# Performance work log

Measured on AMD Instinct MI355X. Metric: run time of the kernel, lower is better.

The kernel has to match this reference:

```python
import jax, jax.numpy as jnp
import numpy as np

B, T, C, H = 4, 4096, 1024, 64  # batch, seq_len, n_embd, head_size


def setup_inputs() -> dict:
    key = jax.random.key(0)
    kx, kk, kq, kv = jax.random.split(key, 4)
    x = jax.random.normal(kx, (B, T, C), dtype=jnp.float32)
    Wk = jax.random.normal(kk, (C, H), dtype=jnp.float32) * (C ** -0.5)
    Wq = jax.random.normal(kq, (C, H), dtype=jnp.float32) * (C ** -0.5)
    Wv = jax.random.normal(kv, (C, H), dtype=jnp.float32) * (C ** -0.5)
    return {"x": x, "Wk": Wk, "Wq": Wq, "Wv": Wv}


def reference(x, Wk, Wq, Wv):
    # q,k,v: (B,T,H)
    k = jnp.einsum('btc,ch->bth', x, Wk)
    q = jnp.einsum('btc,ch->bth', x, Wq)
    v = jnp.einsum('btc,ch->bth', x, Wv)
    # NOTE: source scales by C**-0.5 (embedding dim), not head_size**-0.5
    scale = jnp.asarray(C, x.dtype) ** -0.5
    scores = jnp.einsum('bqh,bkh->bqk', q, k) * scale  # (B,T,T)
    causal = jnp.tril(jnp.ones((T, T), dtype=bool))
    scores = jnp.where(causal, scores, jnp.asarray(-jnp.inf, scores.dtype))
    weight = jax.nn.softmax(scores, axis=-1)
    out = jnp.einsum('bqk,bkh->bqh', weight, v)  # (B,T,H)
    return out
```

## Files before the change

kernel.cpp:

```cpp
#include <hip/hip_runtime.h>

typedef unsigned short u16;
typedef unsigned int u32;
typedef float v4f __attribute__((ext_vector_type(4)));
typedef __bf16 v8bf __attribute__((ext_vector_type(8)));

__device__ __forceinline__ u16 f2bf(float f) {
    union { float f; u32 u; } v; v.f = f;
    u32 r = v.u + 0x7fffu + ((v.u >> 16) & 1u);
    return (u16)(r >> 16);
}
__device__ __forceinline__ u32 pk2(float lo, float hi) {
    return ((u32)f2bf(hi) << 16) | (u32)f2bf(lo);
}
__device__ __forceinline__ u32 pk2t(float lo, float hi) {
    union { float f; u32 u; } a, b; a.f = hi; b.f = lo;
    return __builtin_amdgcn_perm(a.u, b.u, 0x07060302u);
}
__device__ __forceinline__ v4f zero4() { v4f z = {0.f, 0.f, 0.f, 0.f}; return z; }

__global__ __launch_bounds__(64) void prep_w(const float* __restrict__ Wk,
                                             const float* __restrict__ Wq,
                                             const float* __restrict__ Wv,
                                             u16* __restrict__ WtF) {
    const int f = blockIdx.x >> 5;
    const int ks = blockIdx.x & 31;
    const int lane = threadIdx.x;
    const int w = f >> 2;
    const float* W = (w == 0) ? Wk : ((w == 1) ? Wq : Wv);
    const int h = (f & 3) * 16 + (lane & 15);
    const int k0 = ks * 32 + (lane >> 4) * 8;
    u16 tmp[8];
#pragma unroll
    for (int j = 0; j < 8; ++j) tmp[j] = f2bf(W[(size_t)(k0 + j) * 64 + h]);
    *(uint4*)&WtF[((size_t)blockIdx.x * 64 + lane) * 8] = *(const uint4*)tmp;
}

__global__ __launch_bounds__(256, 4) void qkv_proj(const float* __restrict__ x,
                                                   const u16* __restrict__ WtF,
                                                   u16* __restrict__ qg,
                                                   u16* __restrict__ Kf,
                                                   u16* __restrict__ Vf) {
    __shared__ v4f red[3][12][64];
    u16* Tk = (u16*)&red[0][0][0];
    u16* Tq = Tk + 16 * 72;
    u16* Tv = Tq + 16 * 72;

    const int tid = threadIdx.x;
    const int lane = tid & 63;
    const int wv = tid >> 6;
    const int l15 = lane & 15, quad = lane >> 4;
    const int row0 = blockIdx.x * 16;

    v4f acc[12];
#pragma unroll
    for (int i = 0; i < 12; ++i) acc[i] = zero4();

    const float* xr = x + (size_t)(row0 + l15) * 1024 + wv * 256 + quad * 8;

    union { u32 u[4]; v8bf v; } af[8];
#pragma unroll
    for (int half = 0; half < 2; ++half) {
        float4 t[8];
#pragma unroll
        for (int i = 0; i < 8; ++i)
            t[i] = *(const float4*)(xr + half * 128 + (i >> 1) * 32 + (i & 1) * 4);
#pragma unroll
        for (int j = 0; j < 4; ++j) {
            int ks = half * 4 + j;
            af[ks].u[0] = pk2(t[2 * j].x, t[2 * j].y);
            af[ks].u[1] = pk2(t[2 * j].z, t[2 * j].w);
            af[ks].u[2] = pk2(t[2 * j + 1].x, t[2 * j + 1].y);
            af[ks].u[3] = pk2(t[2 * j + 1].z, t[2 * j + 1].w);
        }
    }

    const u16* wf0 = WtF + ((size_t)(wv * 8) * 64 + lane) * 8;
#pragma unroll
    for (int f = 0; f < 12; ++f) {
        const u16* wpf = wf0 + (size_t)f * 16384;
#pragma unroll
        for (int ks = 0; ks < 8; ++ks) {
            acc[f] = __builtin_amdgcn_mfma_f32_16x16x32_bf16(
                af[ks].v, *(const v8bf*)(wpf + ks * 512), acc[f], 0, 0, 0);
        }
    }

    if (wv > 0) {
#pragma unroll
        for (int f = 0; f < 12; ++f) red[wv - 1][f][lane] = acc[f];
    }
    __syncthreads();
    if (wv == 0) {
#pragma unroll
        for (int f = 0; f < 12; ++f) {
            acc[f] += red[0][f][lane];
            acc[f] += red[1][f][lane];
            acc[f] += red[2][f][lane];
        }
    }
    __syncthreads();
    if (wv == 0) {
        const float QSC = 0.04508422002778f;
#pragma unroll
        for (int ct = 0; ct < 4; ++ct)
#pragma unroll
            for (int r = 0; r < 4; ++r) {
                Tk[(quad * 4 + r) * 72 + ct * 16 + l15] = f2bf(acc[ct][r]);
                Tq[(quad * 4 + r) * 72 + ct * 16 + l15] = f2bf(acc[ct + 4][r] * QSC);
                Tv[(ct * 16 + l15) * 24 + quad * 4 + r] = f2bf(acc[ct + 8][r]);
            }
    }
    __syncthreads();

    const int b = row0 >> 12, t0 = row0 & 4095;
    const int kt = t0 >> 6, ctk = (t0 >> 4) & 3, ksv = (t0 >> 5) & 1;
    const int p0q = (t0 & 31) >> 3;

    if (tid < 128) {
        int tok = tid >> 3, h8 = (tid & 7) << 3;
        *(uint4*)&qg[((size_t)(b * 4096 + t0 + tok)) * 64 + h8] =
            *(const uint4*)&Tq[tok * 72 + h8];
        int ht = tid >> 5, sub = (tid >> 4) & 1, l15p = tid & 15;
        int lane2 = (p0q + sub) * 16 + l15p;
        size_t fb = ((((size_t)(b * 64 + kt) * 4 + ht) * 2 + ksv) * 64 + lane2) * 8;
        *(uint4*)&Vf[fb] = *(const uint4*)&Tv[(ht * 16 + l15p) * 24 + sub * 8];
    } else {
        int lam = tid - 128;
        int ks = lam >> 6, ln = lam & 63;
        int l15p = ln & 15, qd = ln >> 4;
        size_t fb = ((((size_t)(b * 64 + kt) * 4 + ctk) * 2 + ks) * 64 + ln) * 8;
        *(uint4*)&Kf[fb] = *(const uint4*)&Tk[l15p * 72 + ks * 32 + qd * 8];
    }
}

__global__ __launch_bounds__(128, 3) void attn_part(const u16* __restrict__ qg,
                                                    const u16* __restrict__ Kf,
                                                    const u16* __restrict__ Vf,
                                                    float* __restrict__ Op,
                                                    float* __restrict__ ml,
                                                    int KC, int MAXCH) {
    const int a = blockIdx.x, c = blockIdx.y, b = blockIdx.z;
    if (c * KC > a) return;

    const int tid  = threadIdx.x;
    const int lane = tid & 63;
    const int wv   = tid >> 6;
    const int l15  = lane & 15;
    const int quad = lane >> 4;
    const int q0   = a * 64 + wv * 32;

    v8bf qf[2][2];
#pragma unroll
    for (int st = 0; st < 2; ++st) {
        const u16* p = qg + ((size_t)(b * 4096 + q0 + st * 16 + l15)) * 64 + quad * 8;
        qf[st][0] = *(const v8bf*)p;
        qf[st][1] = *(const v8bf*)(p + 32);
    }

    union { u32 u[4]; v8bf v; } ones;
    ones.u[0] = ones.u[1] = ones.u[2] = ones.u[3] = 0x3F803F80u;

    v4f o[2][4], l5[2];
#pragma unroll
    for (int st = 0; st < 2; ++st) {
        l5[st] = zero4();
#pragma unroll
        for (int i = 0; i < 4; ++i) o[st][i] = zero4();
    }

    const int kt0 = c * KC;
    const int kt1 = (kt0 + KC < a + 1) ? (kt0 + KC) : (a + 1);

    for (int kt = kt0; kt < kt1; ++kt) {
        const size_t tb = ((size_t)(b * 64 + kt) * 4) * 2 * 512;
        const u16* kp = Kf + tb + lane * 8;
        const u16* vp = Vf + tb + lane * 8;

        v8bf ka[4][2], av[4][2];
#pragma unroll
        for (int ct = 0; ct < 4; ++ct) {
            ka[ct][0] = *(const v8bf*)(kp + (ct * 2 + 0) * 512);
            ka[ct][1] = *(const v8bf*)(kp + (ct * 2 + 1) * 512);
            av[ct][0] = *(const v8bf*)(vp + (ct * 2 + 0) * 512);
            av[ct][1] = *(const v8bf*)(vp + (ct * 2 + 1) * 512);
        }

#pragma unroll
        for (int st = 0; st < 2; ++st) {
            v4f s[4];
#pragma unroll
            for (int ct = 0; ct < 4; ++ct) {
                v4f t = zero4();
                t = __builtin_amdgcn_mfma_f32_16x16x32_bf16(ka[ct][0], qf[st][0], t, 0, 0, 0);
                t = __builtin_amdgcn_mfma_f32_16x16x32_bf16(ka[ct][1], qf[st][1], t, 0, 0, 0);
                s[ct] = t;
            }

            if (kt == a) {
                const int queryg = q0 + st * 16 + l15;
                const int key0 = kt * 64 + quad * 4;
#pragma unroll
                for (int ct = 0; ct < 4; ++ct)
#pragma unroll
                    for (int r = 0; r < 4; ++r)
                        s[ct][r] = ((key0 + ct * 16 + r) > queryg) ? -1e30f : s[ct][r];
            }

            u32 pk[4][2];
#pragma unroll
            for (int ct = 0; ct < 4; ++ct) {
                float p0 = exp2f(s[ct][0]);
                float p1 = exp2f(s[ct][1]);
                float p2 = exp2f(s[ct][2]);
                float p3 = exp2f(s[ct][3]);
                pk[ct][0] = pk2t(p0, p1);
                pk[ct][1] = pk2t(p2, p3);
            }

            const int srcA = ((quad & 1) << 5) + l15;
            const int srcB = srcA + 16;
            const bool hi = (quad >= 2);
#pragma unroll
            for (int ks = 0; ks < 2; ++ks) {
                u32 g0a = (u32)__shfl((int)pk[ks * 2][0], srcA);
                u32 g0b = (u32)__shfl((int)pk[ks * 2 + 1][0], srcA);
                u32 g1a = (u32)__shfl((int)pk[ks * 2][1], srcA);
                u32 g1b = (u32)__shfl((int)pk[ks * 2 + 1][1], srcA);
                u32 g2a = (u32)__shfl((int)pk[ks * 2][0], srcB);
                u32 g2b = (u32)__shfl((int)pk[ks * 2 + 1][0], srcB);
                u32 g3a = (u32)__shfl((int)pk[ks * 2][1], srcB);
                u32 g3b = (u32)__shfl((int)pk[ks * 2 + 1][1], srcB);
                union { u32 u[4]; v8bf v; } pf;
                pf.u[0] = hi ? g0b : g0a;
                pf.u[1] = hi ? g1b : g1a;
                pf.u[2] = hi ? g2b : g2a;
                pf.u[3] = hi ? g3b : g3a;
#pragma unroll
                for (int ht = 0; ht < 4; ++ht)
                    o[st][ht] = __builtin_amdgcn_mfma_f32_16x16x32_bf16(
                        av[ht][ks], pf.v, o[st][ht], 0, 0, 0);
                l5[st] = __builtin_amdgcn_mfma_f32_16x16x32_bf16(
                    ones.v, pf.v, l5[st], 0, 0, 0);
            }
        }
    }

    size_t pidx = ((size_t)b * 64 + a) * MAXCH + c;
    float* op = Op + pidx * 4096;
#pragma unroll
    for (int st = 0; st < 2; ++st) {
#pragma unroll
        for (int ht = 0; ht < 4; ++ht)
#pragma unroll
            for (int r = 0; r < 4; ++r)
                op[(ht * 16 + quad * 4 + r) * 64 + wv * 32 + st * 16 + l15] = o[st][ht][r];
        if (quad == 0)
            ml[pidx * 64 + wv * 32 + st * 16 + l15] = l5[st][0];
    }
}

__global__ __launch_bounds__(256) void attn_combine(const float* __restrict__ Op,
                                                    const float* __restrict__ ml,
                                                    float* __restrict__ out,
                                                    int KC, int MAXCH) {
    const int a = blockIdx.x, b = blockIdx.y, hz = blockIdx.z;
    const int nch = a / KC + 1;
    const int tid = threadIdx.x;
    const int q = tid & 63, hq = tid >> 6;
    const int h0 = hz * 16 + hq * 4;
    const size_t pbase = ((size_t)b * 64 + a) * MAXCH;

    float L = 0.f;
    float acc[4] = {0.f, 0.f, 0.f, 0.f};
    for (int c = 0; c < nch; ++c) {
        L += ml[(pbase + c) * 64 + q];
        const float* op = Op + (pbase + c) * 4096;
#pragma unroll
        for (int j = 0; j < 4; ++j) acc[j] += op[(h0 + j) * 64 + q];
    }
    float inv = 1.f / L;
    float4 st = {acc[0] * inv, acc[1] * inv, acc[2] * inv, acc[3] * inv};
    *(float4*)&out[((size_t)b * 4096 + a * 64 + q) * 64 + h0] = st;
}

extern "C" void kernel_launch(void* const* d_in, const int* in_sizes, int n_in,
                              void* d_out, int out_size, void* d_ws, size_t ws_size,
                              hipStream_t stream) {
    const float* x  = (const float*)d_in[0];
    const float* Wk = (const float*)d_in[1];
    const float* Wq = (const float*)d_in[2];
    const float* Wv = (const float*)d_in[3];
    float* out = (float*)d_out;

    char* wsb = (char*)d_ws;
    u16* WtF = (u16*)wsb;
    u16* qg  = (u16*)(wsb + 393216);
    u16* Kf  = (u16*)(wsb + 393216 + 2097152);
    u16* Vf  = (u16*)(wsb + 393216 + 2 * 2097152);
    const size_t base = 393216 + 3 * 2097152;

    int KC = 8, MAXCH = 8;
    while (KC < 64 && base + (size_t)256 * MAXCH * (4096 + 64) * 4 > ws_size) {
        KC <<= 1; MAXCH >>= 1;
    }
    float* Op = (float*)(wsb + base);
    float* ml = Op + (size_t)256 * MAXCH * 4096;

    prep_w<<<dim3(384), dim3(64), 0, stream>>>(Wk, Wq, Wv, WtF);
    qkv_proj<<<dim3(1024), dim3(256), 0, stream>>>(x, WtF, qg, Kf, Vf);
    attn_part<<<dim3(64, MAXCH, 4), dim3(128), 0, stream>>>(qg, Kf, Vf, Op, ml, KC, MAXCH);
    attn_combine<<<dim3(64, 4, 4), dim3(256), 0, stream>>>(Op, ml, out, KC, MAXCH);
}
```

Before: 143.7 us.

## Store attention partials as packed bf16, pre-fragment Q, and halve key chunk size

Partial attention outputs are now written as bf16 pairs packed into u32 words instead of fp32. This halves the partial-output traffic between attn_part and attn_combine. Q is written by qkv_proj directly in MFMA fragment order, so attn_part loads it with contiguous per-lane reads. The key chunk size drops from 8 to 4 tiles with up to 16 chunks, giving more split-K parallelism for the causal workload at the cost of more partials to combine and some bf16 rounding in the partial sums.

Result: no change. 144.0 us (+0.2%).

```diff
diff --git a/kernel.cpp b/kernel.cpp
--- a/kernel.cpp
+++ b/kernel.cpp
@@ -16,6 +16,12 @@
 __device__ __forceinline__ u32 pk2t(float lo, float hi) {
     union { float f; u32 u; } a, b; a.f = hi; b.f = lo;
     return __builtin_amdgcn_perm(a.u, b.u, 0x07060302u);
+}
+__device__ __forceinline__ float bfLo(u32 p) {
+    union { u32 u; float f; } v; v.u = p << 16; return v.f;
+}
+__device__ __forceinline__ float bfHi(u32 p) {
+    union { u32 u; float f; } v; v.u = p & 0xffff0000u; return v.f;
 }
 __device__ __forceinline__ v4f zero4() { v4f z = {0.f, 0.f, 0.f, 0.f}; return z; }
 
@@ -38,7 +44,7 @@
 
 __global__ __launch_bounds__(256, 4) void qkv_proj(const float* __restrict__ x,
                                                    const u16* __restrict__ WtF,
-                                                   u16* __restrict__ qg,
+                                                   u16* __restrict__ qgf,
                                                    u16* __restrict__ Kf,
                                                    u16* __restrict__ Vf) {
     __shared__ v4f red[3][12][64];
@@ -116,11 +122,12 @@
     const int b = row0 >> 12, t0 = row0 & 4095;
     const int kt = t0 >> 6, ctk = (t0 >> 4) & 3, ksv = (t0 >> 5) & 1;
     const int p0q = (t0 & 31) >> 3;
+    const int g = blockIdx.x;
 
     if (tid < 128) {
-        int tok = tid >> 3, h8 = (tid & 7) << 3;
-        *(uint4*)&qg[((size_t)(b * 4096 + t0 + tok)) * 64 + h8] =
-            *(const uint4*)&Tq[tok * 72 + h8];
+        int f = tid >> 6, ln = tid & 63;
+        *(uint4*)&qgf[((size_t)(g * 2 + f) * 64 + ln) * 8] =
+            *(const uint4*)&Tq[(ln & 15) * 72 + f * 32 + (ln >> 4) * 8];
         int ht = tid >> 5, sub = (tid >> 4) & 1, l15p = tid & 15;
         int lane2 = (p0q + sub) * 16 + l15p;
         size_t fb = ((((size_t)(b * 64 + kt) * 4 + ht) * 2 + ksv) * 64 + lane2) * 8;
@@ -134,10 +141,10 @@
     }
 }
 
-__global__ __launch_bounds__(128, 3) void attn_part(const u16* __restrict__ qg,
+__global__ __launch_bounds__(128, 3) void attn_part(const u16* __restrict__ qgf,
                                                     const u16* __restrict__ Kf,
                                                     const u16* __restrict__ Vf,
-                                                    float* __restrict__ Op,
+                                                    u32* __restrict__ Opb,
                                                     float* __restrict__ ml,
                                                     int KC, int MAXCH) {
     const int a = blockIdx.x, c = blockIdx.y, b = blockIdx.z;
@@ -150,12 +157,13 @@
     const int quad = lane >> 4;
     const int q0   = a * 64 + wv * 32;
 
+    const int g0 = (b * 4096 + q0) >> 4;
     v8bf qf[2][2];
 #pragma unroll
     for (int st = 0; st < 2; ++st) {
-        const u16* p = qg + ((size_t)(b * 4096 + q0 + st * 16 + l15)) * 64 + quad * 8;
-        qf[st][0] = *(const v8bf*)p;
-        qf[st][1] = *(const v8bf*)(p + 32);
+#pragma unroll
+        for (int f = 0; f < 2; ++f)
+            qf[st][f] = *(const v8bf*)&qgf[((size_t)((g0 + st) * 2 + f) * 64 + lane) * 8];
     }
 
     union { u32 u[4]; v8bf v; } ones;
@@ -247,20 +255,21 @@
     }
 
     size_t pidx = ((size_t)b * 64 + a) * MAXCH + c;
-    float* op = Op + pidx * 4096;
+    u32* op = Opb + pidx * 2048;
 #pragma unroll
     for (int st = 0; st < 2; ++st) {
 #pragma unroll
-        for (int ht = 0; ht < 4; ++ht)
+        for (int ht = 0; ht < 2; ++ht)
 #pragma unroll
             for (int r = 0; r < 4; ++r)
-                op[(ht * 16 + quad * 4 + r) * 64 + wv * 32 + st * 16 + l15] = o[st][ht][r];
+                op[(ht * 16 + quad * 4 + r) * 64 + wv * 32 + st * 16 + l15] =
+                    pk2t(o[st][ht][r], o[st][ht + 2][r]);
         if (quad == 0)
             ml[pidx * 64 + wv * 32 + st * 16 + l15] = l5[st][0];
     }
 }
 
-__global__ __launch_bounds__(256) void attn_combine(const float* __restrict__ Op,
+__global__ __launch_bounds__(256) void attn_combine(const u32* __restrict__ Opb,
                                                     const float* __restrict__ ml,
                                                     float* __restrict__ out,
                                                     int KC, int MAXCH) {
@@ -269,15 +278,20 @@
     const int tid = threadIdx.x;
     const int q = tid & 63, hq = tid >> 6;
     const int h0 = hz * 16 + hq * 4;
+    const int rb = h0 & 31;
+    const bool hi = (h0 >= 32);
     const size_t pbase = ((size_t)b * 64 + a) * MAXCH;
 
     float L = 0.f;
     float acc[4] = {0.f, 0.f, 0.f, 0.f};
     for (int c = 0; c < nch; ++c) {
         L += ml[(pbase + c) * 64 + q];
-        const float* op = Op + (pbase + c) * 4096;
-#pragma unroll
-        for (int j = 0; j < 4; ++j) acc[j] += op[(h0 + j) * 64 + q];
+        const u32* op = Opb + (pbase + c) * 2048;
+#pragma unroll
+        for (int j = 0; j < 4; ++j) {
+            u32 v = op[(rb + j) * 64 + q];
+            acc[j] += hi ? bfHi(v) : bfLo(v);
+        }
     }
     float inv = 1.f / L;
     float4 st = {acc[0] * inv, acc[1] * inv, acc[2] * inv, acc[3] * inv};
@@ -295,20 +309,20 @@
 
     char* wsb = (char*)d_ws;
     u16* WtF = (u16*)wsb;
-    u16* qg  = (u16*)(wsb + 393216);
+    u16* qgf = (u16*)(wsb + 393216);
     u16* Kf  = (u16*)(wsb + 393216 + 2097152);
     u16* Vf  = (u16*)(wsb + 393216 + 2 * 2097152);
     const size_t base = 393216 + 3 * 2097152;
 
-    int KC = 8, MAXCH = 8;
-    while (KC < 64 && base + (size_t)256 * MAXCH * (4096 + 64) * 4 > ws_size) {
+    int KC = 4, MAXCH = 16;
+    while (KC < 64 && base + (size_t)256 * MAXCH * (2048 * 4 + 256) > ws_size) {
         KC <<= 1; MAXCH >>= 1;
     }
-    float* Op = (float*)(wsb + base);
-    float* ml = Op + (size_t)256 * MAXCH * 4096;
+    u32* Opb = (u32*)(wsb + base);
+    float* ml = (float*)(wsb + base + (size_t)256 * MAXCH * 2048 * 4);
 
     prep_w<<<dim3(384), dim3(64), 0, stream>>>(Wk, Wq, Wv, WtF);
-    qkv_proj<<<dim3(1024), dim3(256), 0, stream>>>(x, WtF, qg, Kf, Vf);
-    attn_part<<<dim3(64, MAXCH, 4), dim3(128), 0, stream>>>(qg, Kf, Vf, Op, ml, KC, MAXCH);
-    attn_combine<<<dim3(64, 4, 4), dim3(256), 0, stream>>>(Op, ml, out, KC, MAXCH);
-}
+    qkv_proj<<<dim3(1024), dim3(256), 0, stream>>>(x, WtF, qgf, Kf, Vf);
+    attn_part<<<dim3(64, MAXCH, 4), dim3(128), 0, stream>>>(qgf, Kf, Vf, Opb, ml, KC, MAXCH);
+    attn_combine<<<dim3(64, 4, 4), dim3(256), 0, stream>>>(Opb, ml, out, KC, MAXCH);
+}
```
